# Kernel optimization log

Hardware: AMD Instinct MI355X
Metric: run time of the kernel (lower is better)

Reference implementation:

```python
import jax, jax.numpy as jnp
import numpy as np

N, D = 8192, 256
E = 65536


def setup_inputs() -> dict:
    key = jax.random.key(0)
    ks = jax.random.split(key, 16)
    s = 1.0 / np.sqrt(D)  # nn.Linear default init scale
    return {
        "x_mean": jax.random.normal(ks[0], (N, D), dtype=jnp.float32),
        "x_var": jax.random.uniform(ks[1], (N, D), dtype=jnp.float32),
        "edge_index": jax.random.randint(ks[2], (2, E), 0, N, dtype=jnp.int64),
        "edge_timestamps": jax.random.uniform(ks[3], (E,), dtype=jnp.float32),
        "Wq": jax.random.uniform(ks[4], (D, D), jnp.float32, -s, s),
        "bq": jax.random.uniform(ks[5], (D,), jnp.float32, -s, s),
        "Wk": jax.random.uniform(ks[6], (D, D), jnp.float32, -s, s),
        "bk": jax.random.uniform(ks[7], (D,), jnp.float32, -s, s),
        "Wv": jax.random.uniform(ks[8], (D, D), jnp.float32, -s, s),
        "bv": jax.random.uniform(ks[9], (D,), jnp.float32, -s, s),
        "Wo": jax.random.uniform(ks[10], (D, D), jnp.float32, -s, s),
        "bo": jax.random.uniform(ks[11], (D,), jnp.float32, -s, s),
        "Wvar": jax.random.uniform(ks[12], (D, D), jnp.float32, -s, s),
        "bvar": jax.random.uniform(ks[13], (D,), jnp.float32, -s, s),
    }


def reference(x_mean, x_var, edge_index, edge_timestamps,
              Wq, bq, Wk, bk, Wv, bv, Wo, bo, Wvar, bvar):
    # edge_index / edge_timestamps are accepted but unused (as in the original forward).
    head_dim = D // 4  # num_heads=4; heads are never split, only used for scale
    scale = head_dim ** -0.5

    q = x_mean @ Wq.T + bq  # [N, D]
    k = x_mean @ Wk.T + bk
    v = x_mean @ Wv.T + bv

    attn = jax.nn.softmax((q @ k.T) * scale, axis=-1)  # [N, N] (dropout: eval mode)

    out_mean = (attn @ v) @ Wo.T + bo  # [N, D]

    v_var = x_var @ Wvar.T + bvar
    out_var = (attn * attn) @ v_var  # squared weights against projected variance
    return out_mean, out_var
```

## Files before the change

kernel.cpp:

```cpp
#include <hip/hip_runtime.h>
#include <hip/hip_bf16.h>
#include <hip/hip_fp16.h>

#define DEV __device__ __forceinline__

typedef __attribute__((ext_vector_type(8))) _Float16 h8;
typedef __attribute__((ext_vector_type(4))) float floatx4;

DEV float bf2f(unsigned short b) { return __uint_as_float(((unsigned)b) << 16); }

DEV void async_ld16(const void* g, void* l) {
  __builtin_amdgcn_global_load_lds(
      (const __attribute__((address_space(1))) unsigned int*)g,
      (__attribute__((address_space(3))) unsigned int*)l, 16, 0, 0);
}

DEV int detect_bf16(const void* x_mean) {
  const unsigned* w = (const unsigned*)x_mean;
  unsigned v = w[threadIdx.x & 63];
  unsigned ex = (v >> 7) & 0xFFu;
  int vote = (ex >= 100u && ex <= 144u) ? 1 : 0;
  unsigned long long b = __ballot(vote);
  return __popcll(b) >= 48 ? 1 : 0;
}

DEV float load_elem(const void* p, int isbf, size_t i) {
  return isbf ? bf2f(((const unsigned short*)p)[i]) : ((const float*)p)[i];
}

DEV void stage8h(const void* src, int isbf, size_t idx, float scale, _Float16* dst) {
  h8 o;
  if (isbf) {
    const unsigned short* s = (const unsigned short*)src + idx;
#pragma unroll
    for (int j = 0; j < 8; ++j) o[j] = (_Float16)(bf2f(s[j]) * scale);
  } else {
    const float* f = (const float*)src + idx;
    float4 a = *(const float4*)f;
    float4 b = *(const float4*)(f + 4);
    o[0] = (_Float16)(a.x * scale); o[1] = (_Float16)(a.y * scale);
    o[2] = (_Float16)(a.z * scale); o[3] = (_Float16)(a.w * scale);
    o[4] = (_Float16)(b.x * scale); o[5] = (_Float16)(b.y * scale);
    o[6] = (_Float16)(b.z * scale); o[7] = (_Float16)(b.w * scale);
  }
  *(h8*)dst = o;
}

struct ProjArgs {
  const void* A[4];
  const void* B[4];
  const void* bias[4];
  _Float16* C[4];
  int fl_tpc[4];
  float scale[4];
  int bias_row[4];
  const void* xdet;
};

__global__ __launch_bounds__(256) void proj_kernel(ProjArgs p) {
  __shared__ __align__(16) char smem[34816];
  _Float16* As = (_Float16*)smem;
  _Float16* Bs = As + 4096;
  _Float16* Ts = (_Float16*)smem;
  int isbf = detect_bf16(p.xdet);
  int z = blockIdx.z;
  size_t i0, j0;
  if (z < 2) { i0 = (size_t)blockIdx.x * 128; j0 = (size_t)blockIdx.y * 128; }
  else       { i0 = (size_t)blockIdx.y * 128; j0 = (size_t)blockIdx.x * 128; }
  const void* A = p.A[z];
  const void* B = p.B[z];
  const void* bias = p.bias[z];
  const float scale = p.scale[z];
  const int bias_row = p.bias_row[z];
  const int tpc = p.fl_tpc[z];
  _Float16* C = p.C[z];
  const int t = threadIdx.x;
  const int lane = t & 63, wave = t >> 6;
  const int wr = wave >> 1, wc = wave & 1;
  const int q = lane >> 4, m = lane & 15;
  floatx4 acc[4][4] = {};
  for (int k0 = 0; k0 < 256; k0 += 32) {
#pragma unroll
    for (int it = 0; it < 2; ++it) {
      int e = it * 2048 + t * 8;
      int row = e >> 5, col = e & 31;
      stage8h(A, isbf, (i0 + row) * (size_t)256 + k0 + col, 1.f, &As[e]);
      stage8h(B, isbf, (j0 + row) * (size_t)256 + k0 + col, 1.f, &Bs[e]);
    }
    __syncthreads();
    h8 af[4], bfr[4];
#pragma unroll
    for (int r = 0; r < 4; ++r)
      af[r] = *(const h8*)&As[(wr * 64 + r * 16 + m) * 32 + q * 8];
#pragma unroll
    for (int c = 0; c < 4; ++c)
      bfr[c] = *(const h8*)&Bs[(wc * 64 + c * 16 + m) * 32 + q * 8];
#pragma unroll
    for (int r = 0; r < 4; ++r)
#pragma unroll
      for (int c = 0; c < 4; ++c)
        acc[r][c] = __builtin_amdgcn_mfma_f32_16x16x32_f16(af[r], bfr[c], acc[r][c], 0, 0, 0);
    __syncthreads();
  }
#pragma unroll
  for (int r = 0; r < 4; ++r)
#pragma unroll
    for (int c = 0; c < 4; ++c) {
      size_t col = j0 + wc * 64 + c * 16 + m;
      float bcol = bias_row ? 0.f : load_elem(bias, isbf, col);
#pragma unroll
      for (int g = 0; g < 4; ++g) {
        size_t row = i0 + wr * 64 + r * 16 + q * 4 + g;
        float val = acc[r][c][g] + bcol;
        if (bias_row) val += load_elem(bias, isbf, row);
        Ts[(wr * 64 + r * 16 + q * 4 + g) * 136 + wc * 64 + c * 16 + m] =
            (_Float16)(val * scale);
      }
    }
  __syncthreads();
  size_t ti0 = i0 >> 4, tj0 = j0 >> 5;
#pragma unroll
  for (int it = 0; it < 8; ++it) {
    int cch = it * 4 + wave;
    int ci = cch >> 2, ck = cch & 3;
    int il = ci * 16 + (lane & 15);
    int jl = ck * 32 + (lane >> 4) * 8;
    h8 v = *(const h8*)&Ts[il * 136 + jl];
    *(h8*)&C[((ti0 + ci) * (size_t)tpc + (tj0 + ck)) * 512 + lane * 8] = v;
  }
}

__global__ __launch_bounds__(256) void zero_rs_kernel(float* __restrict__ rs) {
  rs[blockIdx.x * 256 + threadIdx.x] = 0.f;
}
__global__ __launch_bounds__(256) void zero_acc_kernel(float* __restrict__ a,
                                                       float* __restrict__ b) {
  size_t i = ((size_t)blockIdx.x * 256 + threadIdx.x) * 4;
  float4 z = {0.f, 0.f, 0.f, 0.f};
  *(float4*)(a + i) = z;
  *(float4*)(b + i) = z;
}

__global__ __launch_bounds__(512, 4) void flash_kernel(
    const _Float16* __restrict__ qb, const _Float16* __restrict__ kb,
    const _Float16* __restrict__ vT, const _Float16* __restrict__ vvT,
    float* __restrict__ rs, float* __restrict__ otm, float* __restrict__ otv) {
  __shared__ __align__(16) _Float16 Qs[32 * 512];
  __shared__ __align__(16) _Float16 Ks[32 * 512];
  __shared__ __align__(16) _Float16 Ps[16 * 512];
  const int t = threadIdx.x;
  const int lane = t & 63, wave = t >> 6;
  const int hi = lane >> 4, m = lane & 15;
  const size_t bx = blockIdx.x;
  const int z = blockIdx.y;
  const int wq = wave >> 2, wk = wave & 3;
  const int wq2 = wave >> 2, wd = wave & 3;

#pragma unroll
  for (int it = 0; it < 4; ++it) {
    int tile = it * 8 + wave;
    async_ld16(&qb[((bx * 4 + (size_t)(tile >> 3)) * 8 + (tile & 7)) * 512 + lane * 8],
               &Qs[tile * 512 + lane * 8]);
  }
  floatx4 accm[2][4] = {}, accv[2][4] = {};
  float rsum[2][4] = {};
  const size_t kvRowBase = (size_t)z * 128;
  for (int kvt = 0; kvt < 16; ++kvt) {
    floatx4 s[2][2] = {};
    const size_t kvRow0 = kvRowBase + kvt * 8;
#pragma unroll
    for (int ko = 0; ko < 2; ++ko) {
#pragma unroll
      for (int it = 0; it < 4; ++it)
        async_ld16(&kb[((kvRow0 + wave) * 8 + (size_t)(ko * 4 + it)) * 512 + lane * 8],
                   &Ks[(wave * 4 + it) * 512 + lane * 8]);
      __syncthreads();
#pragma unroll
      for (int kt2 = 0; kt2 < 4; ++kt2) {
        h8 af[2], bf[2];
#pragma unroll
        for (int r = 0; r < 2; ++r)
          af[r] = *(const h8*)&Qs[((wq * 2 + r) * 8 + ko * 4 + kt2) * 512 + lane * 8];
#pragma unroll
        for (int c = 0; c < 2; ++c)
          bf[c] = *(const h8*)&Ks[((wk * 2 + c) * 4 + kt2) * 512 + lane * 8];
#pragma unroll
        for (int r = 0; r < 2; ++r)
#pragma unroll
          for (int c = 0; c < 2; ++c)
            s[r][c] = __builtin_amdgcn_mfma_f32_16x16x32_f16(af[r], bf[c], s[r][c], 0, 0, 0);
      }
      __syncthreads();
    }
#pragma unroll
    for (int r = 0; r < 2; ++r)
#pragma unroll
      for (int c = 0; c < 2; ++c) {
        int lp = hi * 4 + 16 * (2 * c + (m >> 3));
        _Float16* dst = &Ps[((wq * 2 + r) * 4 + wk) * 512 + lp * 8 + (m & 7)];
#pragma unroll
        for (int g = 0; g < 4; ++g) {
          float e = __expf(fminf(s[r][c][g], 8.f)) * 0.015625f;
          rsum[r][g] += e;
          dst[g * 8] = (_Float16)e;
        }
      }
    __syncthreads();
    const size_t kvT0 = (size_t)z * 64 + kvt * 4;
#pragma unroll
    for (int ks = 0; ks < 4; ++ks) {
      h8 a[2], b1[4];
#pragma unroll
      for (int c = 0; c < 4; ++c)
        b1[c] = *(const h8*)&vT[((size_t)(wd * 4 + c) * 256 + kvT0 + ks) * 512 + lane * 8];
#pragma unroll
      for (int r = 0; r < 2; ++r)
        a[r] = *(const h8*)&Ps[((wq2 * 2 + r) * 4 + ks) * 512 + lane * 8];
#pragma unroll
      for (int r = 0; r < 2; ++r)
#pragma unroll
        for (int c = 0; c < 4; ++c)
          accm[r][c] = __builtin_amdgcn_mfma_f32_16x16x32_f16(a[r], b1[c], accm[r][c], 0, 0, 0);
    }
#pragma unroll
    for (int ks = 0; ks < 4; ++ks) {
      h8 a2[2], b2[4];
#pragma unroll
      for (int c = 0; c < 4; ++c)
        b2[c] = *(const h8*)&vvT[((size_t)(wd * 4 + c) * 256 + kvT0 + ks) * 512 + lane * 8];
#pragma unroll
      for (int r = 0; r < 2; ++r) {
        h8 a = *(const h8*)&Ps[((wq2 * 2 + r) * 4 + ks) * 512 + lane * 8];
        a2[r] = a * a;
      }
#pragma unroll
      for (int r = 0; r < 2; ++r)
#pragma unroll
        for (int c = 0; c < 4; ++c)
          accv[r][c] = __builtin_amdgcn_mfma_f32_16x16x32_f16(a2[r], b2[c], accv[r][c], 0, 0, 0);
    }
  }
#pragma unroll
  for (int r = 0; r < 2; ++r)
#pragma unroll
    for (int g = 0; g < 4; ++g) {
      float part = rsum[r][g];
      part += __shfl_xor(part, 1);
      part += __shfl_xor(part, 2);
      part += __shfl_xor(part, 4);
      part += __shfl_xor(part, 8);
      if (m == 0)
        unsafeAtomicAdd(&rs[bx * 64 + wq * 32 + r * 16 + hi * 4 + g], part);
    }
#pragma unroll
  for (int r = 0; r < 2; ++r)
#pragma unroll
    for (int g = 0; g < 4; ++g) {
      size_t row = bx * 64 + wq2 * 32 + r * 16 + hi * 4 + g;
#pragma unroll
      for (int c = 0; c < 4; ++c) {
        size_t col = wd * 64 + c * 16 + m;
        unsafeAtomicAdd(&otm[row * 256 + col], accm[r][c][g]);
        unsafeAtomicAdd(&otv[row * 256 + col], accv[r][c][g]);
      }
    }
}

__global__ __launch_bounds__(256) void final_kernel(const float* __restrict__ ot,
                                                    const void* Wo, const void* bo,
                                                    const void* xdet,
                                                    const float* __restrict__ rs,
                                                    float* __restrict__ Cm,
                                                    float* __restrict__ otv) {
  __shared__ __align__(16) _Float16 As[64 * 32];
  __shared__ __align__(16) _Float16 Bs[128 * 32];
  int isbf = detect_bf16(xdet);
  const int t = threadIdx.x;
  const int lane = t & 63, wave = t >> 6;
  const int wr = wave >> 1, wc = wave & 1;
  const int q = lane >> 4, m = lane & 15;
  const size_t i0 = (size_t)blockIdx.x * 64, j0 = (size_t)blockIdx.y * 128;
  floatx4 acc[2][4] = {};
  for (int k0 = 0; k0 < 256; k0 += 32) {
    {
      int e = t * 8;
      int row = e >> 5, col = e & 31;
      stage8h(ot, 0, (i0 + row) * (size_t)256 + k0 + col, 1.f, &As[e]);
    }
#pragma unroll
    for (int it = 0; it < 2; ++it) {
      int e = it * 2048 + t * 8;
      int row = e >> 5, col = e & 31;
      stage8h(Wo, isbf, (j0 + row) * (size_t)256 + k0 + col, 1.f, &Bs[e]);
    }
    __syncthreads();
    h8 af[2], bfr[4];
#pragma unroll
    for (int r = 0; r < 2; ++r)
      af[r] = *(const h8*)&As[(wr * 32 + r * 16 + m) * 32 + q * 8];
#pragma unroll
    for (int c = 0; c < 4; ++c)
      bfr[c] = *(const h8*)&Bs[(wc * 64 + c * 16 + m) * 32 + q * 8];
#pragma unroll
    for (int r = 0; r < 2; ++r)
#pragma unroll
      for (int c = 0; c < 4; ++c)
        acc[r][c] = __builtin_amdgcn_mfma_f32_16x16x32_f16(af[r], bfr[c], acc[r][c], 0, 0, 0);
    __syncthreads();
  }
#pragma unroll
  for (int r = 0; r < 2; ++r)
#pragma unroll
    for (int g = 0; g < 4; ++g) {
      size_t row = i0 + wr * 32 + r * 16 + q * 4 + g;
      float inv = 1.f / rs[row];
#pragma unroll
      for (int c = 0; c < 4; ++c) {
        size_t col = j0 + wc * 64 + c * 16 + m;
        float bcol = load_elem(bo, isbf, col);
        Cm[row * 256 + col] = acc[r][c][g] * inv + bcol;
      }
    }
#pragma unroll
  for (int it = 0; it < 8; ++it) {
    int e = it * 256 + t;
    int row = e >> 5, cg = e & 31;
    size_t rrow = i0 + row;
    float inv = 1.f / rs[rrow];
    float inv2 = inv * inv;
    float4* pp = (float4*)&otv[rrow * 256 + j0 + cg * 4];
    float4 v = *pp;
    v.x *= inv2; v.y *= inv2; v.z *= inv2; v.w *= inv2;
    *pp = v;
  }
}

extern "C" void kernel_launch(void* const* d_in, const int* in_sizes, int n_in,
                              void* d_out, int out_size, void* d_ws, size_t ws_size,
                              hipStream_t stream) {
  const void* x_mean = d_in[0];
  const void* x_var  = d_in[1];
  const void* Wq   = d_in[4];
  const void* bq   = d_in[5];
  const void* Wk   = d_in[6];
  const void* bk   = d_in[7];
  const void* Wv   = d_in[8];
  const void* bv   = d_in[9];
  const void* Wo   = d_in[10];
  const void* bo   = d_in[11];
  const void* Wvar = d_in[12];
  const void* bvar = d_in[13];
  float* out = (float*)d_out;

  const size_t NE_S = 67108864;
  const size_t NE_P = 2097152;
  if (ws_size < (NE_S + 5 * NE_P) * 2) return;
  _Float16* w   = (_Float16*)d_ws;
  _Float16* qb  = w;
  _Float16* kb  = qb + NE_P;
  _Float16* vT  = kb + NE_P;
  _Float16* vvT = vT + NE_P;
  float* rs     = (float*)(vvT + NE_P);
  float* ot_f32 = rs + 8192;

  ProjArgs p;
  p.A[0] = x_mean; p.B[0] = Wq;     p.bias[0] = bq;   p.C[0] = qb;  p.fl_tpc[0] = 8;   p.scale[0] = 0.125f; p.bias_row[0] = 0;
  p.A[1] = x_mean; p.B[1] = Wk;     p.bias[1] = bk;   p.C[1] = kb;  p.fl_tpc[1] = 8;   p.scale[1] = 1.f;    p.bias_row[1] = 0;
  p.A[2] = Wv;     p.B[2] = x_mean; p.bias[2] = bv;   p.C[2] = vT;  p.fl_tpc[2] = 256; p.scale[2] = 1.f;    p.bias_row[2] = 1;
  p.A[3] = Wvar;   p.B[3] = x_var;  p.bias[3] = bvar; p.C[3] = vvT; p.fl_tpc[3] = 256; p.scale[3] = 1.f;    p.bias_row[3] = 1;
  p.xdet = x_mean;

  zero_rs_kernel<<<dim3(32), 256, 0, stream>>>(rs);
  zero_acc_kernel<<<dim3(2048), 256, 0, stream>>>(ot_f32, out + NE_P);
  proj_kernel<<<dim3(64, 2, 4), 256, 0, stream>>>(p);
  flash_kernel<<<dim3(128, 4), 512, 0, stream>>>(qb, kb, vT, vvT, rs, ot_f32, out + NE_P);
  final_kernel<<<dim3(128, 2), 256, 0, stream>>>(ot_f32, Wo, bo, x_mean, rs, out, out + NE_P);
}
```

Measured before the change: 336.2 us.

## Replace atomic split-K accumulation with per-split partial buffers and XCD-aware block mapping

The flash kernel no longer atomically adds its partial output tiles into zeroed global accumulators. Each of the four KV splits now writes plain stores into its own partial buffer, and the final kernel sums the four partials while staging and scaling. This removes the zero-fill kernel and the contention on float atomics, at the cost of four times the workspace and extra reads in the final kernel. The flash grid is also flattened to 1D with a mapping that places blocks sharing a KV split on the same XCD, so their K/V data stays in that XCD's L2.

```diff
diff --git a/kernel.cpp b/kernel.cpp
--- a/kernel.cpp
+++ b/kernel.cpp
@@ -133,26 +133,22 @@
 __global__ __launch_bounds__(256) void zero_rs_kernel(float* __restrict__ rs) {
   rs[blockIdx.x * 256 + threadIdx.x] = 0.f;
 }
-__global__ __launch_bounds__(256) void zero_acc_kernel(float* __restrict__ a,
-                                                       float* __restrict__ b) {
-  size_t i = ((size_t)blockIdx.x * 256 + threadIdx.x) * 4;
-  float4 z = {0.f, 0.f, 0.f, 0.f};
-  *(float4*)(a + i) = z;
-  *(float4*)(b + i) = z;
-}
 
 __global__ __launch_bounds__(512, 4) void flash_kernel(
     const _Float16* __restrict__ qb, const _Float16* __restrict__ kb,
     const _Float16* __restrict__ vT, const _Float16* __restrict__ vvT,
-    float* __restrict__ rs, float* __restrict__ otm, float* __restrict__ otv) {
+    float* __restrict__ rs, float* __restrict__ otm4, float* __restrict__ otv4) {
   __shared__ __align__(16) _Float16 Qs[32 * 512];
   __shared__ __align__(16) _Float16 Ks[32 * 512];
   __shared__ __align__(16) _Float16 Ps[16 * 512];
+  const size_t NP = 2097152;
   const int t = threadIdx.x;
   const int lane = t & 63, wave = t >> 6;
   const int hi = lane >> 4, m = lane & 15;
-  const size_t bx = blockIdx.x;
-  const int z = blockIdx.y;
+  const int wid = blockIdx.x;
+  const int xcd = wid & 7;
+  const int z = xcd >> 1;
+  const size_t bx = (size_t)((xcd & 1) * 64 + (wid >> 3));
   const int wq = wave >> 2, wk = wave & 3;
   const int wq2 = wave >> 2, wd = wave & 3;
 
@@ -252,6 +248,8 @@
       if (m == 0)
         unsafeAtomicAdd(&rs[bx * 64 + wq * 32 + r * 16 + hi * 4 + g], part);
     }
+  float* om = otm4 + (size_t)z * NP;
+  float* ov = otv4 + (size_t)z * NP;
 #pragma unroll
   for (int r = 0; r < 2; ++r)
 #pragma unroll
@@ -260,20 +258,22 @@
 #pragma unroll
       for (int c = 0; c < 4; ++c) {
         size_t col = wd * 64 + c * 16 + m;
-        unsafeAtomicAdd(&otm[row * 256 + col], accm[r][c][g]);
-        unsafeAtomicAdd(&otv[row * 256 + col], accv[r][c][g]);
-      }
-    }
-}
-
-__global__ __launch_bounds__(256) void final_kernel(const float* __restrict__ ot,
+        om[row * 256 + col] = accm[r][c][g];
+        ov[row * 256 + col] = accv[r][c][g];
+      }
+    }
+}
+
+__global__ __launch_bounds__(256) void final_kernel(const float* __restrict__ ot4,
                                                     const void* Wo, const void* bo,
                                                     const void* xdet,
                                                     const float* __restrict__ rs,
+                                                    const float* __restrict__ otv4,
                                                     float* __restrict__ Cm,
-                                                    float* __restrict__ otv) {
+                                                    float* __restrict__ Cv) {
   __shared__ __align__(16) _Float16 As[64 * 32];
   __shared__ __align__(16) _Float16 Bs[128 * 32];
+  const size_t NP = 2097152;
   int isbf = detect_bf16(xdet);
   const int t = threadIdx.x;
   const int lane = t & 63, wave = t >> 6;
@@ -285,7 +285,20 @@
     {
       int e = t * 8;
       int row = e >> 5, col = e & 31;
-      stage8h(ot, 0, (i0 + row) * (size_t)256 + k0 + col, 1.f, &As[e]);
+      size_t idx = (i0 + row) * (size_t)256 + k0 + col;
+      h8 o;
+#pragma unroll
+      for (int h = 0; h < 2; ++h) {
+        float4 a0 = *(const float4*)&ot4[idx + h * 4];
+        float4 a1 = *(const float4*)&ot4[NP + idx + h * 4];
+        float4 a2 = *(const float4*)&ot4[2 * NP + idx + h * 4];
+        float4 a3 = *(const float4*)&ot4[3 * NP + idx + h * 4];
+        o[h * 4 + 0] = (_Float16)(a0.x + a1.x + a2.x + a3.x);
+        o[h * 4 + 1] = (_Float16)(a0.y + a1.y + a2.y + a3.y);
+        o[h * 4 + 2] = (_Float16)(a0.z + a1.z + a2.z + a3.z);
+        o[h * 4 + 3] = (_Float16)(a0.w + a1.w + a2.w + a3.w);
+      }
+      *(h8*)&As[t * 8] = o;
     }
 #pragma unroll
     for (int it = 0; it < 2; ++it) {
@@ -328,10 +341,17 @@
     size_t rrow = i0 + row;
     float inv = 1.f / rs[rrow];
     float inv2 = inv * inv;
-    float4* pp = (float4*)&otv[rrow * 256 + j0 + cg * 4];
-    float4 v = *pp;
-    v.x *= inv2; v.y *= inv2; v.z *= inv2; v.w *= inv2;
-    *pp = v;
+    size_t o = rrow * 256 + j0 + cg * 4;
+    float4 v0 = *(const float4*)&otv4[o];
+    float4 v1 = *(const float4*)&otv4[NP + o];
+    float4 v2 = *(const float4*)&otv4[2 * NP + o];
+    float4 v3 = *(const float4*)&otv4[3 * NP + o];
+    float4 v;
+    v.x = (v0.x + v1.x + v2.x + v3.x) * inv2;
+    v.y = (v0.y + v1.y + v2.y + v3.y) * inv2;
+    v.z = (v0.z + v1.z + v2.z + v3.z) * inv2;
+    v.w = (v0.w + v1.w + v2.w + v3.w) * inv2;
+    *(float4*)&Cv[o] = v;
   }
 }
 
@@ -361,7 +381,8 @@
   _Float16* vT  = kb + NE_P;
   _Float16* vvT = vT + NE_P;
   float* rs     = (float*)(vvT + NE_P);
-  float* ot_f32 = rs + 8192;
+  float* otm4   = rs + 8192;
+  float* otv4   = otm4 + 4 * NE_P;
 
   ProjArgs p;
   p.A[0] = x_mean; p.B[0] = Wq;     p.bias[0] = bq;   p.C[0] = qb;  p.fl_tpc[0] = 8;   p.scale[0] = 0.125f; p.bias_row[0] = 0;
@@ -371,8 +392,7 @@
   p.xdet = x_mean;
 
   zero_rs_kernel<<<dim3(32), 256, 0, stream>>>(rs);
-  zero_acc_kernel<<<dim3(2048), 256, 0, stream>>>(ot_f32, out + NE_P);
   proj_kernel<<<dim3(64, 2, 4), 256, 0, stream>>>(p);
-  flash_kernel<<<dim3(128, 4), 512, 0, stream>>>(qb, kb, vT, vvT, rs, ot_f32, out + NE_P);
-  final_kernel<<<dim3(128, 2), 256, 0, stream>>>(ot_f32, Wo, bo, x_mean, rs, out, out + NE_P);
-}
+  flash_kernel<<<dim3(512), 512, 0, stream>>>(qb, kb, vT, vvT, rs, otm4, otv4);
+  final_kernel<<<dim3(128, 2), 256, 0, stream>>>(otm4, Wo, bo, x_mean, rs, otv4, out, out + NE_P);
+}
```

New measurement: 324.4 us. 3.5% less time.
